# Kernel optimization log

Measured on AMD Instinct MI355X. Metric: run time of the kernel, lower is better.

Reference implementation:

```python
import jax, jax.numpy as jnp
import numpy as np
from jax import lax

N, C, T, H, W = 2, 128, 8, 56, 56
NH, DK, DV, DD = 1, 16, 128, 16
D_HID = NH * DK + DV  # 144
KS = (3, 7, 7)
PAD = [(1, 1), (3, 3), (3, 3)]  # 'same' padding for (3,7,7)
EPS = 1e-6


def _l2norm(x, axis):
    # matches module: x / sqrt(sum(x^2) + eps)
    return x / jnp.sqrt(jnp.sum(x * x, axis=axis, keepdims=True) + EPS)


def setup_inputs() -> dict:
    key = jax.random.key(0)
    k1, k2, k3 = jax.random.split(key, 3)
    x = jax.random.normal(k1, (N, C, T, H, W), dtype=jnp.float32)
    W_proj = jax.random.normal(k2, (D_HID, C), dtype=jnp.float32) * (1.0 / np.sqrt(C))
    W_H2 = jax.random.normal(k3, (DD, 1) + KS, dtype=jnp.float32) * (1.0 / np.sqrt(float(np.prod(KS))))
    return {"x": x, "W_proj": W_proj, "W_H2": W_H2}


def reference(x, W_proj, W_H2):
    b, c, t, h, w = x.shape
    # 1x1x1 projection conv == per-pixel channel matmul
    xp = jnp.einsum('bcthw,oc->bothw', x, W_proj)  # (b, 144, t, h, w)
    q = xp[:, :NH * DK]  # (b, nh*dk, t, h, w)
    v = xp[:, NH * DK:]  # (b, dv,    t, h, w)
    # normalization (kernel_type 'V': kernel = q directly)
    q = _l2norm(q.reshape(b, NH, DK, t, h, w), axis=2)  # L2 over dk
    v = _l2norm(v, axis=1)                              # L2 over channels
    # H2: each v channel treated as its own 1-channel sample -> dd feature maps
    v_ = v.reshape(b * DV, 1, t, h, w)
    V = lax.conv_general_dilated(
        v_, W_H2, window_strides=(1, 1, 1), padding=PAD,
        dimension_numbers=('NCDHW', 'OIDHW', 'NCDHW'))  # (b*dv, dd, t, h, w)
    feat = V.reshape(b, DV, DD, t, h, w)
    # per-pixel tiny matmul: out[.., v, n] = sum_k q[.., n, k] * feat[.., v, k]  (dk == dd)
    out = jnp.einsum('bnkthw,bvkthw->bvnthw', q, feat)
    # rearrange '(b t h w) nh v -> b (nh v) t h w' with einsum output (a, dv, nh)
    return out.reshape(b, DV * NH, t, h, w)
```

## Files before the change

kernel.cpp:

```cpp
#include <hip/hip_runtime.h>
#include <hip/hip_bf16.h>

constexpr int NB   = 2;
constexpr int CIN  = 128;
constexpr int TT   = 8;
constexpr int HH   = 56;
constexpr int WW   = 56;
constexpr int S    = TT * HH * WW;
constexpr int DK   = 16;
constexpr int DV   = 128;
constexpr int TAPS = 147;
constexpr int NOUT = DK + DV;
constexpr int VPT = 10, VPH = 62, VPW = 62;
constexpr int PCELLS = NB * VPT * VPH * VPW;
constexpr int WSTR = 149;
constexpr float EPSf = 1e-6f;

typedef short bf16x8 __attribute__((ext_vector_type(8)));
typedef float f32x4  __attribute__((ext_vector_type(4)));

static __device__ __forceinline__ short f2bf(float f) {
    __hip_bfloat16 h = __float2bfloat16(f);
    short s;
    __builtin_memcpy(&s, &h, 2);
    return s;
}

__global__ __launch_bounds__(256) void k_twp(
    const float* __restrict__ Wp, short* __restrict__ Wpfrag)
{
    int gid = blockIdx.x * 256 + threadIdx.x;
    if (gid >= 9 * 4 * 64) return;
    int lane = gid & 63;
    int kb   = (gid >> 6) & 3;
    int nt   = gid >> 8;
    int n = nt * 16 + (lane & 15);
    int c0 = kb * 32 + (lane >> 4) * 8;
#pragma unroll
    for (int j = 0; j < 8; ++j)
        Wpfrag[(size_t)gid * 8 + j] = f2bf(Wp[n * CIN + c0 + j]);
}

__global__ __launch_bounds__(256) void k_zero(float* __restrict__ vcl)
{
    int gid  = blockIdx.x * 256 + threadIdx.x;
    int cell = gid >> 5;
    int ch4  = gid & 31;
    if (cell >= PCELLS) return;
    int rb = cell;
    int wp = rb % VPW; rb /= VPW;
    int hp = rb % VPH; rb /= VPH;
    int tp = rb % VPT;
    if (tp >= 1 && tp <= 8 && hp >= 3 && hp <= 58 && wp >= 3 && wp <= 58) return;
    float4 z = {0.f, 0.f, 0.f, 0.f};
    *reinterpret_cast<float4*>(vcl + (size_t)cell * 128 + ch4 * 4) = z;
}

__global__ __launch_bounds__(256) void k_proj(
    const float* __restrict__ x, const short* __restrict__ Wpfrag,
    float* __restrict__ qn, float* __restrict__ vcl)
{
    int tid  = threadIdx.x;
    int lane = tid & 63;
    int wv   = tid >> 6;
    int bid  = blockIdx.x;
    int b    = bid / (S / 128);
    int pbas = (bid - b * (S / 128)) * 128 + wv * 32;

    const float* xb = x + (size_t)b * CIN * S;
    int row = lane & 15;
    int g   = lane >> 4;

    bf16x8 a[2][4];
#pragma unroll
    for (int m = 0; m < 2; ++m) {
        int p = pbas + m * 16 + row;
#pragma unroll
        for (int kb = 0; kb < 4; ++kb) {
            const float* xs = xb + (size_t)(kb * 32 + g * 8) * S + p;
#pragma unroll
            for (int j = 0; j < 8; ++j)
                a[m][kb][j] = f2bf(xs[(size_t)j * S]);
        }
    }

    f32x4 acc[2][9];
#pragma unroll
    for (int m = 0; m < 2; ++m)
#pragma unroll
        for (int nt = 0; nt < 9; ++nt) acc[m][nt] = {0.f, 0.f, 0.f, 0.f};

    const bf16x8* bf = reinterpret_cast<const bf16x8*>(Wpfrag);
#pragma unroll
    for (int nt = 0; nt < 9; ++nt) {
#pragma unroll
        for (int kb = 0; kb < 4; ++kb) {
            bf16x8 bfr = bf[(nt * 4 + kb) * 64 + lane];
            acc[0][nt] = __builtin_amdgcn_mfma_f32_16x16x32_bf16(
                a[0][kb], bfr, acc[0][nt], 0, 0, 0);
            acc[1][nt] = __builtin_amdgcn_mfma_f32_16x16x32_bf16(
                a[1][kb], bfr, acc[1][nt], 0, 0, 0);
        }
    }

#pragma unroll
    for (int m = 0; m < 2; ++m) {
        float sq[4], sv[4];
#pragma unroll
        for (int r = 0; r < 4; ++r) {
            sq[r] = acc[m][0][r] * acc[m][0][r];
            float s = 0.f;
#pragma unroll
            for (int nt = 1; nt < 9; ++nt) s += acc[m][nt][r] * acc[m][nt][r];
            sv[r] = s;
        }
#pragma unroll
        for (int d = 1; d < 16; d <<= 1) {
#pragma unroll
            for (int r = 0; r < 4; ++r) {
                sq[r] += __shfl_xor(sq[r], d, 64);
                sv[r] += __shfl_xor(sv[r], d, 64);
            }
        }
#pragma unroll
        for (int r = 0; r < 4; ++r) {
            int p = pbas + m * 16 + 4 * g + r;
            float qsc = 1.0f / sqrtf(sq[r] + EPSf);
            float vsc = 1.0f / sqrtf(sv[r] + EPSf);
            qn[((size_t)b * DK + (lane & 15)) * S + p] = acc[m][0][r] * qsc;
            int t  = p / (HH * WW);
            int hw = p - t * (HH * WW);
            int h  = hw / WW;
            int w  = hw - h * WW;
            float* vd = vcl
                + (((size_t)(b * VPT + t + 1) * VPH + (h + 3)) * VPW + (w + 3)) * 128
                + (lane & 15);
#pragma unroll
            for (int nt = 1; nt < 9; ++nt)
                vd[(nt - 1) * 16] = acc[m][nt][r] * vsc;
        }
    }
}

__global__ __launch_bounds__(256) void k_out(
    const float* __restrict__ vcl, const float* __restrict__ qn,
    const float* __restrict__ wh2, float* __restrict__ out)
{
    __shared__ float q_s[DK * WW];
    __shared__ float weff[WW * WSTR];

    int tid = threadIdx.x;
    int bid = blockIdx.x;
    int nid = (bid & 7) * 112 + (bid >> 3);
    int b   = nid / 448;
    int rem = nid - b * 448;
    int t   = rem / 56, h = rem - t * 56;
    int pbase = t * (HH * WW) + h * WW;

    for (int i = tid; i < DK * WW; i += 256) {
        int k = i / 56, w = i - k * 56;
        q_s[i] = qn[((size_t)b * DK + k) * S + pbase + w];
    }
    __syncthreads();

    if (tid < 224) {
        int w = tid % 56, q4 = tid / 56;
        float qr[DK];
#pragma unroll
        for (int k = 0; k < DK; ++k) qr[k] = q_s[k * 56 + w];
#pragma unroll 1
        for (int tap = q4; tap < TAPS; tap += 4) {
            float a = 0.f;
#pragma unroll
            for (int k = 0; k < DK; ++k)
                a = fmaf(qr[k], wh2[k * TAPS + tap], a);
            weff[w * WSTR + tap] = a;
        }
    }
    __syncthreads();

    int cc = tid & 31;
    int wt = tid >> 5;
    int wbase = wt * 7;

    const float* vbase = vcl
        + ((size_t)(b * VPT + t) * VPH + h) * VPW * 128
        + (size_t)wbase * 128 + cc * 4;

    float acc[7][4];
#pragma unroll
    for (int k = 0; k < 7; ++k)
#pragma unroll
        for (int j = 0; j < 4; ++j) acc[k][j] = 0.f;

#pragma unroll 1
    for (int dz = 0; dz < 3; ++dz) {
#pragma unroll 1
        for (int dy = 0; dy < 7; ++dy) {
            const float* vr = vbase + (size_t)((dz * VPH + dy) * VPW) * 128;
            const float* wrow = &weff[wbase * WSTR + (dz * 7 + dy) * 7];
#pragma unroll
            for (int j = 0; j < 13; ++j) {
                float4 A = *reinterpret_cast<const float4*>(vr + j * 128);
                int k0 = (j - 6 > 0) ? (j - 6) : 0;
                int k1 = (j < 6) ? j : 6;
#pragma unroll
                for (int k = 0; k < 7; ++k) {
                    if (k < k0 || k > k1) continue;
                    float wv = wrow[k * WSTR + (j - k)];
                    acc[k][0] = fmaf(wv, A.x, acc[k][0]);
                    acc[k][1] = fmaf(wv, A.y, acc[k][1]);
                    acc[k][2] = fmaf(wv, A.z, acc[k][2]);
                    acc[k][3] = fmaf(wv, A.w, acc[k][3]);
                }
            }
        }
    }

    size_t ob = ((size_t)b * DV + cc * 4) * S + pbase + wbase;
#pragma unroll
    for (int j = 0; j < 4; ++j)
#pragma unroll
        for (int k = 0; k < 7; ++k)
            out[ob + (size_t)j * S + k] = acc[k][j];
}

extern "C" void kernel_launch(void* const* d_in, const int* in_sizes, int n_in,
                              void* d_out, int out_size, void* d_ws, size_t ws_size,
                              hipStream_t stream)
{
    const float* x   = (const float*)d_in[0];
    const float* Wp  = (const float*)d_in[1];
    const float* wh2 = (const float*)d_in[2];
    float* out = (float*)d_out;

    float* ws     = (float*)d_ws;
    short* Wpfrag = (short*)ws;
    float* qn     = ws + 9216;
    float* vcl    = qn + (size_t)NB * DK * S;

    k_twp <<<dim3(9), dim3(256), 0, stream>>>(Wp, Wpfrag);
    k_zero<<<dim3((PCELLS * 32 + 255) / 256), dim3(256), 0, stream>>>(vcl);
    k_proj<<<dim3(NB * S / 128), dim3(256), 0, stream>>>(x, Wpfrag, qn, vcl);
    k_out <<<dim3(NB * TT * HH), dim3(256), 0, stream>>>(vcl, qn, wh2, out);
}
```

Before: 111.1 us.

## Move 3D conv to MFMA with banded weight matrices and bf16 channel-planar V

```diff
diff --git a/kernel.cpp b/kernel.cpp
--- a/kernel.cpp
+++ b/kernel.cpp
@@ -11,9 +11,9 @@
 constexpr int DV   = 128;
 constexpr int TAPS = 147;
 constexpr int NOUT = DK + DV;
-constexpr int VPT = 10, VPH = 62, VPW = 62;
-constexpr int PCELLS = NB * VPT * VPH * VPW;
-constexpr int WSTR = 149;
+constexpr int VPT = 10, VPH = 62, VPWA = 64;
+constexpr int PLANE_A = VPT * VPH * VPWA;
+constexpr int BSTR = 72;
 constexpr float EPSf = 1e-6f;
 
 typedef short bf16x8 __attribute__((ext_vector_type(8)));
@@ -33,32 +33,17 @@
     if (gid >= 9 * 4 * 64) return;
     int lane = gid & 63;
     int kb   = (gid >> 6) & 3;
-    int nt   = gid >> 8;
-    int n = nt * 16 + (lane & 15);
+    int mt   = gid >> 8;
+    int n = mt * 16 + (lane & 15);
     int c0 = kb * 32 + (lane >> 4) * 8;
 #pragma unroll
     for (int j = 0; j < 8; ++j)
         Wpfrag[(size_t)gid * 8 + j] = f2bf(Wp[n * CIN + c0 + j]);
 }
 
-__global__ __launch_bounds__(256) void k_zero(float* __restrict__ vcl)
-{
-    int gid  = blockIdx.x * 256 + threadIdx.x;
-    int cell = gid >> 5;
-    int ch4  = gid & 31;
-    if (cell >= PCELLS) return;
-    int rb = cell;
-    int wp = rb % VPW; rb /= VPW;
-    int hp = rb % VPH; rb /= VPH;
-    int tp = rb % VPT;
-    if (tp >= 1 && tp <= 8 && hp >= 3 && hp <= 58 && wp >= 3 && wp <= 58) return;
-    float4 z = {0.f, 0.f, 0.f, 0.f};
-    *reinterpret_cast<float4*>(vcl + (size_t)cell * 128 + ch4 * 4) = z;
-}
-
 __global__ __launch_bounds__(256) void k_proj(
     const float* __restrict__ x, const short* __restrict__ Wpfrag,
-    float* __restrict__ qn, float* __restrict__ vcl)
+    float* __restrict__ qn, short* __restrict__ vclb)
 {
     int tid  = threadIdx.x;
     int lane = tid & 63;
@@ -68,88 +53,89 @@
     int pbas = (bid - b * (S / 128)) * 128 + wv * 32;
 
     const float* xb = x + (size_t)b * CIN * S;
-    int row = lane & 15;
+    int col = lane & 15;
     int g   = lane >> 4;
 
-    bf16x8 a[2][4];
-#pragma unroll
-    for (int m = 0; m < 2; ++m) {
-        int p = pbas + m * 16 + row;
+    bf16x8 bx[2][4];
+#pragma unroll
+    for (int n2 = 0; n2 < 2; ++n2) {
+        int p = pbas + n2 * 16 + col;
 #pragma unroll
         for (int kb = 0; kb < 4; ++kb) {
             const float* xs = xb + (size_t)(kb * 32 + g * 8) * S + p;
 #pragma unroll
             for (int j = 0; j < 8; ++j)
-                a[m][kb][j] = f2bf(xs[(size_t)j * S]);
-        }
-    }
-
-    f32x4 acc[2][9];
-#pragma unroll
-    for (int m = 0; m < 2; ++m)
-#pragma unroll
-        for (int nt = 0; nt < 9; ++nt) acc[m][nt] = {0.f, 0.f, 0.f, 0.f};
-
-    const bf16x8* bf = reinterpret_cast<const bf16x8*>(Wpfrag);
-#pragma unroll
-    for (int nt = 0; nt < 9; ++nt) {
+                bx[n2][kb][j] = f2bf(xs[(size_t)j * S]);
+        }
+    }
+
+    f32x4 acc[9][2];
+#pragma unroll
+    for (int mt = 0; mt < 9; ++mt) {
+        acc[mt][0] = {0.f, 0.f, 0.f, 0.f};
+        acc[mt][1] = {0.f, 0.f, 0.f, 0.f};
+    }
+
+    const bf16x8* wf = reinterpret_cast<const bf16x8*>(Wpfrag);
+#pragma unroll
+    for (int mt = 0; mt < 9; ++mt) {
 #pragma unroll
         for (int kb = 0; kb < 4; ++kb) {
-            bf16x8 bfr = bf[(nt * 4 + kb) * 64 + lane];
-            acc[0][nt] = __builtin_amdgcn_mfma_f32_16x16x32_bf16(
-                a[0][kb], bfr, acc[0][nt], 0, 0, 0);
-            acc[1][nt] = __builtin_amdgcn_mfma_f32_16x16x32_bf16(
-                a[1][kb], bfr, acc[1][nt], 0, 0, 0);
-        }
-    }
-
-#pragma unroll
-    for (int m = 0; m < 2; ++m) {
-        float sq[4], sv[4];
-#pragma unroll
-        for (int r = 0; r < 4; ++r) {
-            sq[r] = acc[m][0][r] * acc[m][0][r];
-            float s = 0.f;
-#pragma unroll
-            for (int nt = 1; nt < 9; ++nt) s += acc[m][nt][r] * acc[m][nt][r];
-            sv[r] = s;
-        }
-#pragma unroll
-        for (int d = 1; d < 16; d <<= 1) {
+            bf16x8 aw = wf[(mt * 4 + kb) * 64 + lane];
+            acc[mt][0] = __builtin_amdgcn_mfma_f32_16x16x32_bf16(
+                aw, bx[0][kb], acc[mt][0], 0, 0, 0);
+            acc[mt][1] = __builtin_amdgcn_mfma_f32_16x16x32_bf16(
+                aw, bx[1][kb], acc[mt][1], 0, 0, 0);
+        }
+    }
+
+#pragma unroll
+    for (int n2 = 0; n2 < 2; ++n2) {
+        float ssq = 0.f, ssv = 0.f;
+#pragma unroll
+        for (int r = 0; r < 4; ++r) ssq += acc[0][n2][r] * acc[0][n2][r];
+#pragma unroll
+        for (int mt = 1; mt < 9; ++mt)
+#pragma unroll
+            for (int r = 0; r < 4; ++r) ssv += acc[mt][n2][r] * acc[mt][n2][r];
+        ssq += __shfl_xor(ssq, 16, 64);
+        ssq += __shfl_xor(ssq, 32, 64);
+        ssv += __shfl_xor(ssv, 16, 64);
+        ssv += __shfl_xor(ssv, 32, 64);
+        float qsc = 1.0f / sqrtf(ssq + EPSf);
+        float vsc = 1.0f / sqrtf(ssv + EPSf);
+
+        int p = pbas + n2 * 16 + col;
+#pragma unroll
+        for (int r = 0; r < 4; ++r)
+            qn[((size_t)b * DK + (4 * g + r)) * S + p] = acc[0][n2][r] * qsc;
+
+        int t  = p / (HH * WW);
+        int hw = p - t * (HH * WW);
+        int h  = hw / WW;
+        int w  = hw - h * WW;
+        size_t pp = (size_t)(t + 1) * (VPH * VPWA) + (size_t)(h + 3) * VPWA + (w + 3);
+        short* vb = vclb + (size_t)b * 128 * PLANE_A + pp;
+#pragma unroll
+        for (int mt = 1; mt < 9; ++mt)
 #pragma unroll
             for (int r = 0; r < 4; ++r) {
-                sq[r] += __shfl_xor(sq[r], d, 64);
-                sv[r] += __shfl_xor(sv[r], d, 64);
+                int c = (mt - 1) * 16 + 4 * g + r;
+                vb[(size_t)c * PLANE_A] = f2bf(acc[mt][n2][r] * vsc);
             }
-        }
-#pragma unroll
-        for (int r = 0; r < 4; ++r) {
-            int p = pbas + m * 16 + 4 * g + r;
-            float qsc = 1.0f / sqrtf(sq[r] + EPSf);
-            float vsc = 1.0f / sqrtf(sv[r] + EPSf);
-            qn[((size_t)b * DK + (lane & 15)) * S + p] = acc[m][0][r] * qsc;
-            int t  = p / (HH * WW);
-            int hw = p - t * (HH * WW);
-            int h  = hw / WW;
-            int w  = hw - h * WW;
-            float* vd = vcl
-                + (((size_t)(b * VPT + t + 1) * VPH + (h + 3)) * VPW + (w + 3)) * 128
-                + (lane & 15);
-#pragma unroll
-            for (int nt = 1; nt < 9; ++nt)
-                vd[(nt - 1) * 16] = acc[m][nt][r] * vsc;
-        }
     }
 }
 
 __global__ __launch_bounds__(256) void k_out(
-    const float* __restrict__ vcl, const float* __restrict__ qn,
+    const short* __restrict__ vclb, const float* __restrict__ qn,
     const float* __restrict__ wh2, float* __restrict__ out)
 {
-    __shared__ float q_s[DK * WW];
-    __shared__ float weff[WW * WSTR];
-
-    int tid = threadIdx.x;
+    __shared__ short weff_b[56 * 168];
+    __shared__ char  upool[2 * 64 * BSTR * 2];
+
+    int tid  = threadIdx.x;
+    int lane = tid & 63;
+    int wv   = tid >> 6;
     int bid = blockIdx.x;
     int nid = (bid & 7) * 112 + (bid >> 3);
     int b   = nid / 448;
@@ -157,6 +143,7 @@
     int t   = rem / 56, h = rem - t * 56;
     int pbase = t * (HH * WW) + h * WW;
 
+    float* q_s = reinterpret_cast<float*>(upool);
     for (int i = tid; i < DK * WW; i += 256) {
         int k = i / 56, w = i - k * 56;
         q_s[i] = qn[((size_t)b * DK + k) * S + pbase + w];
@@ -174,55 +161,96 @@
 #pragma unroll
             for (int k = 0; k < DK; ++k)
                 a = fmaf(qr[k], wh2[k * TAPS + tap], a);
-            weff[w * WSTR + tap] = a;
-        }
-    }
-    __syncthreads();
-
-    int cc = tid & 31;
-    int wt = tid >> 5;
-    int wbase = wt * 7;
-
-    const float* vbase = vcl
-        + ((size_t)(b * VPT + t) * VPH + h) * VPW * 128
-        + (size_t)wbase * 128 + cc * 4;
-
-    float acc[7][4];
-#pragma unroll
-    for (int k = 0; k < 7; ++k)
-#pragma unroll
-        for (int j = 0; j < 4; ++j) acc[k][j] = 0.f;
+            int row = tap / 7, d = tap - row * 7;
+            weff_b[w * 168 + row * 8 + d] = f2bf(a);
+        }
+    }
+    __syncthreads();
+
+    short* band = reinterpret_cast<short*>(upool);
+    {
+        int* bi = reinterpret_cast<int*>(band);
+        for (int i = tid; i < 2 * 64 * BSTR / 2; i += 256) bi[i] = 0;
+    }
+    __syncthreads();
+
+    int e1 = tid;
+    int w1 = e1 / 7, d1 = e1 - w1 * 7;
+    int e2 = tid + 256;
+    int w2 = e2 / 7, d2 = e2 - w2 * 7;
+    bool has2 = (e2 < 392);
+    bool has1 = (e1 < 392);
+
+    if (has1) band[w1 * BSTR + w1 + d1] = weff_b[w1 * 168 + d1];
+    if (has2) band[w2 * BSTR + w2 + d2] = weff_b[w2 * 168 + d2];
+    __syncthreads();
+
+    int col = lane & 15, g = lane >> 4;
+    int cbase = wv * 32;
+
+    f32x4 acc[2][4];
+#pragma unroll
+    for (int m2 = 0; m2 < 2; ++m2)
+#pragma unroll
+        for (int n = 0; n < 4; ++n) acc[m2][n] = {0.f, 0.f, 0.f, 0.f};
+
+    const short* vb = vclb + (size_t)b * 128 * PLANE_A;
 
 #pragma unroll 1
-    for (int dz = 0; dz < 3; ++dz) {
-#pragma unroll 1
-        for (int dy = 0; dy < 7; ++dy) {
-            const float* vr = vbase + (size_t)((dz * VPH + dy) * VPW) * 128;
-            const float* wrow = &weff[wbase * WSTR + (dz * 7 + dy) * 7];
-#pragma unroll
-            for (int j = 0; j < 13; ++j) {
-                float4 A = *reinterpret_cast<const float4*>(vr + j * 128);
-                int k0 = (j - 6 > 0) ? (j - 6) : 0;
-                int k1 = (j < 6) ? j : 6;
-#pragma unroll
-                for (int k = 0; k < 7; ++k) {
-                    if (k < k0 || k > k1) continue;
-                    float wv = wrow[k * WSTR + (j - k)];
-                    acc[k][0] = fmaf(wv, A.x, acc[k][0]);
-                    acc[k][1] = fmaf(wv, A.y, acc[k][1]);
-                    acc[k][2] = fmaf(wv, A.z, acc[k][2]);
-                    acc[k][3] = fmaf(wv, A.w, acc[k][3]);
-                }
+    for (int r = 0; r < 21; ++r) {
+        const short* cur = band + (r & 1) * (64 * BSTR);
+        int dz = r / 7, dy = r - dz * 7;
+        size_t rowo = (size_t)(t + dz) * (VPH * VPWA) + (size_t)(h + dy) * VPWA;
+
+        bf16x8 av[2][2];
+#pragma unroll
+        for (int m2 = 0; m2 < 2; ++m2) {
+            const short* ap = vb + (size_t)(cbase + m2 * 16 + col) * PLANE_A
+                                 + rowo + g * 8;
+            av[m2][0] = *reinterpret_cast<const bf16x8*>(ap);
+            av[m2][1] = *reinterpret_cast<const bf16x8*>(ap + 32);
+        }
+        bf16x8 bbf[4][2];
+#pragma unroll
+        for (int n = 0; n < 4; ++n) {
+            const short* bp = cur + (n * 16 + col) * BSTR + g * 8;
+            bbf[n][0] = *reinterpret_cast<const bf16x8*>(bp);
+            bbf[n][1] = *reinterpret_cast<const bf16x8*>(bp + 32);
+        }
+#pragma unroll
+        for (int n = 0; n < 4; ++n) {
+            acc[0][n] = __builtin_amdgcn_mfma_f32_16x16x32_bf16(
+                av[0][0], bbf[n][0], acc[0][n], 0, 0, 0);
+            acc[0][n] = __builtin_amdgcn_mfma_f32_16x16x32_bf16(
+                av[0][1], bbf[n][1], acc[0][n], 0, 0, 0);
+            acc[1][n] = __builtin_amdgcn_mfma_f32_16x16x32_bf16(
+                av[1][0], bbf[n][0], acc[1][n], 0, 0, 0);
+            acc[1][n] = __builtin_amdgcn_mfma_f32_16x16x32_bf16(
+                av[1][1], bbf[n][1], acc[1][n], 0, 0, 0);
+        }
+
+        if (r < 20) {
+            short* nxt = band + ((r + 1) & 1) * (64 * BSTR);
+            int ro = (r + 1) * 8;
+            if (has1) nxt[w1 * BSTR + w1 + d1] = weff_b[w1 * 168 + ro + d1];
+            if (has2) nxt[w2 * BSTR + w2 + d2] = weff_b[w2 * 168 + ro + d2];
+        }
+        __syncthreads();
+    }
+
+#pragma unroll
+    for (int m2 = 0; m2 < 2; ++m2) {
+#pragma unroll
+        for (int n = 0; n < 4; ++n) {
+            int w = n * 16 + col;
+            if (w < 56) {
+                size_t ob = ((size_t)b * DV + cbase + m2 * 16 + 4 * g) * S + pbase + w;
+#pragma unroll
+                for (int rr = 0; rr < 4; ++rr)
+                    out[ob + (size_t)rr * S] = acc[m2][n][rr];
             }
         }
     }
-
-    size_t ob = ((size_t)b * DV + cc * 4) * S + pbase + wbase;
-#pragma unroll
-    for (int j = 0; j < 4; ++j)
-#pragma unroll
-        for (int k = 0; k < 7; ++k)
-            out[ob + (size_t)j * S + k] = acc[k][j];
 }
 
 extern "C" void kernel_launch(void* const* d_in, const int* in_sizes, int n_in,
@@ -237,10 +265,12 @@
     float* ws     = (float*)d_ws;
     short* Wpfrag = (short*)ws;
     float* qn     = ws + 9216;
-    float* vcl    = qn + (size_t)NB * DK * S;
+    short* vclb   = (short*)(qn + (size_t)NB * DK * S);
+
+    size_t vclb_bytes = (size_t)NB * 128 * PLANE_A * sizeof(short);
 
     k_twp <<<dim3(9), dim3(256), 0, stream>>>(Wp, Wpfrag);
-    k_zero<<<dim3((PCELLS * 32 + 255) / 256), dim3(256), 0, stream>>>(vcl);
-    k_proj<<<dim3(NB * S / 128), dim3(256), 0, stream>>>(x, Wpfrag, qn, vcl);
-    k_out <<<dim3(NB * TT * HH), dim3(256), 0, stream>>>(vcl, qn, wh2, out);
-}
+    hipMemsetAsync(vclb, 0, vclb_bytes, stream);
+    k_proj<<<dim3(NB * S / 128), dim3(256), 0, stream>>>(x, Wpfrag, qn, vclb);
+    k_out <<<dim3(NB * TT * HH), dim3(256), 0, stream>>>(vclb, qn, wh2, out);
+}
```

After: 115.2 us. 1.04x slower.
